# Kernel optimization log

Measured on AMD Instinct MI355X. Metric: run time of the kernel, lower is better.

The kernel has to match this reference:

```python
import jax, jax.numpy as jnp
import numpy as np

T, N, E = 2048, 11, 110
NF, EF, HID, EED, HEADS = 5, 4, 256, 32, 4
D1 = 64 * HEADS  # gat1 output dim = 256
BN_EPS = 1e-5
LN_EPS = 1e-5


def _gat(x, ea, src, dst, W, b, Wa, ba):
    """FallbackGAT: linear, gather src/dst, edge-score, softmax over ALL edges, scatter-add."""
    h = x @ W + b                                             # (N, D)
    sh, dh = h[src], h[dst]                                   # (E, D) gathers
    logits = jnp.concatenate([sh, dh, ea], axis=-1) @ Wa + ba # (E,)
    alpha = jax.nn.softmax(logits)                            # softmax over dim=0 (all edges), as in source
    return jax.ops.segment_sum(alpha[:, None] * sh, dst, num_segments=x.shape[0])


def _forward(x, edge_attr, event_embs, hx, edge_index,
             W_np, b_np, bn_g, bn_b,
             We1, be1, We2, be2,
             Wg1, bg1, Wa1, ba1,
             Wg2, bg2, Wa2, ba2,
             ln_g, ln_b,
             W_ih, W_hh, b_ih, b_hh,
             Wf, bf, Wp1, bp1, Wp2, bp2):
    src, dst = edge_index[0], edge_index[1]
    bn_inv = 1.0 / jnp.sqrt(1.0 + BN_EPS)  # eval-mode BatchNorm with running stats (0, 1)

    def step(h_state, inp):
        xt, eat, evt = inp  # (N,NF), (E,EF), (EED,)
        # node_proj: Linear -> ReLU -> BatchNorm1d (eval)
        h = jax.nn.relu(xt @ W_np + b_np)
        h = bn_g * (h * bn_inv) + bn_b
        # edge_proj: Linear -> ReLU -> Linear -> ReLU
        ea = jax.nn.relu(jax.nn.relu(eat @ We1 + be1) @ We2 + be2)
        # two GAT layers (dropout p=0)
        x1 = jax.nn.relu(_gat(h, ea, src, dst, Wg1, bg1, Wa1, ba1))
        x2 = jax.nn.relu(_gat(x1, ea, src, dst, Wg2, bg2, Wa2, ba2))
        # LayerNorm
        mu = x2.mean(-1, keepdims=True)
        var = ((x2 - mu) ** 2).mean(-1, keepdims=True)
        x2 = ln_g * (x2 - mu) / jnp.sqrt(var + LN_EPS) + ln_b
        # GRUCell (torch gate order r, z, n)
        gi = x2 @ W_ih + b_ih
        gh = h_state @ W_hh + b_hh
        ir, iz, inn = jnp.split(gi, 3, axis=-1)
        hr, hz, hn = jnp.split(gh, 3, axis=-1)
        r = jax.nn.sigmoid(ir + hr)
        z = jax.nn.sigmoid(iz + hz)
        n = jnp.tanh(inn + r * hn)
        h_new = (1.0 - z) * n + z * h_state
        # event fusion + predictor
        ev = jnp.broadcast_to(evt[None, :], (h_new.shape[0], evt.shape[0]))
        fused = jax.nn.relu(jnp.concatenate([h_new, ev], axis=-1) @ Wf + bf)
        pred = jax.nn.relu(fused @ Wp1 + bp1) @ Wp2 + bp2  # (N, 1)
        return h_new, pred

    _, preds = jax.lax.scan(step, hx, (x, edge_attr, event_embs))
    return preds  # (T, N, 1)


def setup_inputs() -> dict:
    key = jax.random.key(0)
    ks = jax.random.split(key, 20)
    def p(i, shape):
        return jax.random.normal(ks[i], shape, dtype=jnp.float32) * 0.05
    return dict(
        x=jax.random.normal(ks[0], (T, N, NF), dtype=jnp.float32),
        edge_attr=jax.random.uniform(ks[1], (T, E, EF), dtype=jnp.float32),
        event_embs=jax.random.normal(ks[2], (T, EED), dtype=jnp.float32),
        hx=jnp.zeros((N, HID), jnp.float32),
        edge_index=jax.random.randint(ks[3], (2, E), 0, N),
        W_np=p(4, (NF, 64)), b_np=jnp.zeros((64,), jnp.float32),
        bn_g=jnp.ones((64,), jnp.float32), bn_b=jnp.zeros((64,), jnp.float32),
        We1=p(5, (EF, 32)), be1=jnp.zeros((32,), jnp.float32),
        We2=p(6, (32, 16)), be2=jnp.zeros((16,), jnp.float32),
        Wg1=p(7, (64, D1)), bg1=jnp.zeros((D1,), jnp.float32),
        Wa1=p(8, (2 * D1 + 16,)), ba1=jnp.zeros((), jnp.float32),
        Wg2=p(9, (D1, HID)), bg2=jnp.zeros((HID,), jnp.float32),
        Wa2=p(10, (2 * HID + 16,)), ba2=jnp.zeros((), jnp.float32),
        ln_g=jnp.ones((HID,), jnp.float32), ln_b=jnp.zeros((HID,), jnp.float32),
        W_ih=p(11, (HID, 3 * HID)), W_hh=p(12, (HID, 3 * HID)),
        b_ih=jnp.zeros((3 * HID,), jnp.float32), b_hh=jnp.zeros((3 * HID,), jnp.float32),
        Wf=p(13, (HID + EED, HID)), bf=jnp.zeros((HID,), jnp.float32),
        Wp1=p(14, (HID, HID // 2)), bp1=jnp.zeros((HID // 2,), jnp.float32),
        Wp2=p(15, (HID // 2, 1)), bp2=jnp.zeros((1,), jnp.float32),
    )


def reference(x, edge_attr, event_embs, hx, edge_index,
              W_np, b_np, bn_g, bn_b,
              We1, be1, We2, be2,
              Wg1, bg1, Wa1, ba1,
              Wg2, bg2, Wa2, ba2,
              ln_g, ln_b,
              W_ih, W_hh, b_ih, b_hh,
              Wf, bf, Wp1, bp1, Wp2, bp2):
    return _forward(x, edge_attr, event_embs, hx, edge_index,
                    W_np, b_np, bn_g, bn_b,
                    We1, be1, We2, be2,
                    Wg1, bg1, Wa1, ba1,
                    Wg2, bg2, Wa2, ba2,
                    ln_g, ln_b,
                    W_ih, W_hh, b_ih, b_hh,
                    Wf, bf, Wp1, bp1, Wp2, bp2)
```

## Files before the change

kernel.cpp:

```cpp
#include <hip/hip_runtime.h>
#include <hip/hip_bf16.h>

#define TT   2048
#define NN   11
#define EE   110
#define NFD  5
#define EFD  4
#define HIDD 256
#define EEDD 32
#define DD1  256
#define G3   768
#define HPAD 264

typedef __attribute__((ext_vector_type(8))) short short8v;
typedef __attribute__((ext_vector_type(4))) float float4v;

static __device__ inline short f2bf(float f) {
    union { __hip_bfloat16 b; short s; } u; u.b = __float2bfloat16(f); return u.s;
}
static __device__ inline float bf2f(short s) {
    union { short s; __hip_bfloat16 b; } u; u.s = s; return __bfloat162float(u.b);
}
static __device__ inline float sigm_f(float x) {
    return __builtin_amdgcn_rcpf(1.f + __builtin_amdgcn_exp2f(-1.4426950408889634f * x));
}
static __device__ inline float tanh_f(float x) {
    float e = __builtin_amdgcn_exp2f(2.8853900817779268f * x);
    return 1.f - 2.f * __builtin_amdgcn_rcpf(e + 1.f);
}
static __device__ inline void gld16(const float* g, float* s) {
    __builtin_amdgcn_global_load_lds((const __attribute__((address_space(1))) void*)g,
                                     (__attribute__((address_space(3))) void*)s, 16, 0, 0);
}

__global__ __launch_bounds__(256) void precompute_kernel(
    const float* __restrict__ x, const float* __restrict__ edge_attr,
    const float* __restrict__ evs, const int* __restrict__ eidx,
    const float* __restrict__ W_np, const float* __restrict__ b_np,
    const float* __restrict__ bn_g, const float* __restrict__ bn_b,
    const float* __restrict__ We1, const float* __restrict__ be1,
    const float* __restrict__ We2, const float* __restrict__ be2,
    const float* __restrict__ Wg1, const float* __restrict__ bg1,
    const float* __restrict__ Wa1, const float* __restrict__ ba1,
    const float* __restrict__ Wg2, const float* __restrict__ bg2,
    const float* __restrict__ Wa2, const float* __restrict__ ba2,
    const float* __restrict__ ln_g, const float* __restrict__ ln_b,
    const float* __restrict__ W_ih, const float* __restrict__ b_ih,
    const float* __restrict__ Wf, const float* __restrict__ bf_,
    float* __restrict__ gi_out, float* __restrict__ evc_out)
{
    const int t   = blockIdx.x;
    const int tid = threadIdx.x;

    __shared__ __align__(16) float sh_h[NN][64];
    __shared__ __align__(16) float sh_e1[EE][32];
    __shared__ __align__(16) float sh_ea[EE][16];
    __shared__ __align__(16) float sh_h1[NN][DD1];
    __shared__ __align__(16) float sh_x[NN][DD1];
    __shared__ float sxt[NN * NFD];
    __shared__ float sev[EEDD];
    __shared__ float seat[EE * EFD];
    __shared__ float red[356];
    __shared__ float sh_s1[NN], sh_d1[NN];
    __shared__ float sh_elog[EE], sh_logit[EE], sh_alpha[EE];
    __shared__ float sh_mu[NN], sh_rs[NN];
    __shared__ float sredv[2];
    __shared__ int s_src[EE], s_dst[EE];
    __shared__ int cnt[NN], deg_start[NN + 1], e_by_dst[EE];

    if (tid < NN * NFD) sxt[tid] = x[(size_t)t * NN * NFD + tid];
    if (tid < EEDD)     sev[tid] = evs[(size_t)t * EEDD + tid];
    for (int i = tid; i < EE * EFD; i += 256)
        seat[i] = edge_attr[(size_t)t * EE * EFD + i];
    if (tid < EE) { s_src[tid] = eidx[tid]; s_dst[tid] = eidx[EE + tid]; }
    if (tid < NN) cnt[tid] = 0;
    __syncthreads();
    if (tid < EE) atomicAdd(&cnt[s_dst[tid]], 1);
    __syncthreads();
    if (tid == 0) {
        int a = 0;
        for (int n = 0; n < NN; n++) { deg_start[n] = a; a += cnt[n]; }
        deg_start[NN] = a;
    }
    __syncthreads();
    if (tid < NN) cnt[tid] = 0;
    __syncthreads();
    if (tid < EE) {
        int d = s_dst[tid];
        int pos = deg_start[d] + atomicAdd(&cnt[d], 1);
        e_by_dst[pos] = tid;
    }

    const float bn_inv = 1.0f / sqrtf(1.0f + 1e-5f);
    __syncthreads();
    for (int i = tid; i < NN * 64; i += 256) {
        int n = i >> 6, d = i & 63;
        float a = b_np[d];
        #pragma unroll
        for (int k = 0; k < NFD; k++) a += sxt[n * NFD + k] * W_np[k * 64 + d];
        a = fmaxf(a, 0.f);
        sh_h[n][d] = bn_g[d] * (a * bn_inv) + bn_b[d];
    }
    __syncthreads();

    for (int i = tid; i < EE * 32; i += 256) {
        int e = i >> 5, d = i & 31;
        float a = be1[d];
        #pragma unroll
        for (int k = 0; k < EFD; k++) a += seat[e * EFD + k] * We1[k * 32 + d];
        sh_e1[e][d] = fmaxf(a, 0.f);
    }
    __syncthreads();
    for (int i = tid; i < EE * 16; i += 256) {
        int e = i >> 4, d = i & 15;
        float a = be2[d];
        #pragma unroll
        for (int k = 0; k < 32; k++) a += sh_e1[e][k] * We2[k * 16 + d];
        sh_ea[e][d] = fmaxf(a, 0.f);
    }
    __syncthreads();

    {
        const int j = tid;
        float acc[NN];
        #pragma unroll
        for (int n = 0; n < NN; n++) acc[n] = bg1[j];
        for (int k = 0; k < 64; k += 4) {
            float w0 = Wg1[(k + 0) * DD1 + j], w1 = Wg1[(k + 1) * DD1 + j];
            float w2 = Wg1[(k + 2) * DD1 + j], w3 = Wg1[(k + 3) * DD1 + j];
            #pragma unroll
            for (int n = 0; n < NN; n++) {
                float4 hv = *(const float4*)&sh_h[n][k];
                acc[n] = fmaf(hv.w, w3, fmaf(hv.z, w2, fmaf(hv.y, w1, fmaf(hv.x, w0, acc[n]))));
            }
        }
        #pragma unroll
        for (int n = 0; n < NN; n++) sh_h1[n][j] = acc[n];
    }
    __syncthreads();
    if (tid < EE) {
        float a = ba1[0];
        #pragma unroll
        for (int k = 0; k < 16; k++) a += sh_ea[tid][k] * Wa1[2 * DD1 + k];
        sh_elog[tid] = a;
    }
    if (tid < 176) {
        int g = tid >> 3, jj = tid & 7;
        int n = (g < NN) ? g : (g - NN);
        const float* wa = (g < NN) ? Wa1 : (Wa1 + DD1);
        float s = 0.f;
        for (int k = jj; k < DD1; k += 8) s += sh_h1[n][k] * wa[k];
        red[tid] = s;
    }
    __syncthreads();
    if (tid < 22) {
        float s = 0.f;
        #pragma unroll
        for (int j2 = 0; j2 < 8; j2++) s += red[tid * 8 + j2];
        if (tid < NN) sh_s1[tid] = s; else sh_d1[tid - NN] = s;
    }
    __syncthreads();
    if (tid < EE) sh_logit[tid] = sh_s1[s_src[tid]] + sh_d1[s_dst[tid]] + sh_elog[tid];
    __syncthreads();
    if (tid < 128) red[tid] = (tid < EE) ? sh_logit[tid] : -3.0e38f;
    __syncthreads();
    for (int s = 64; s > 0; s >>= 1) {
        if (tid < s) red[tid] = fmaxf(red[tid], red[tid + s]);
        __syncthreads();
    }
    if (tid == 0) sredv[0] = red[0];
    __syncthreads();
    if (tid < 128) {
        float v = (tid < EE) ? expf(sh_logit[tid] - sredv[0]) : 0.f;
        if (tid < EE) sh_alpha[tid] = v;
        red[tid] = v;
    }
    __syncthreads();
    for (int s = 64; s > 0; s >>= 1) {
        if (tid < s) red[tid] += red[tid + s];
        __syncthreads();
    }
    if (tid == 0) sredv[1] = 1.f / red[0];
    __syncthreads();
    if (tid < EE) sh_alpha[tid] *= sredv[1];
    __syncthreads();
    for (int i = tid; i < NN * DD1; i += 256) {
        int n = i >> 8, d = i & 255;
        float a = 0.f;
        for (int p = deg_start[n]; p < deg_start[n + 1]; p++) {
            int e = e_by_dst[p];
            a += sh_alpha[e] * sh_h1[s_src[e]][d];
        }
        sh_x[n][d] = fmaxf(a, 0.f);
    }
    __syncthreads();

    {
        const int j = tid;
        float acc[NN];
        #pragma unroll
        for (int n = 0; n < NN; n++) acc[n] = bg2[j];
        for (int k = 0; k < DD1; k += 4) {
            float w0 = Wg2[(k + 0) * DD1 + j], w1 = Wg2[(k + 1) * DD1 + j];
            float w2 = Wg2[(k + 2) * DD1 + j], w3 = Wg2[(k + 3) * DD1 + j];
            #pragma unroll
            for (int n = 0; n < NN; n++) {
                float4 xv = *(const float4*)&sh_x[n][k];
                acc[n] = fmaf(xv.w, w3, fmaf(xv.z, w2, fmaf(xv.y, w1, fmaf(xv.x, w0, acc[n]))));
            }
        }
        #pragma unroll
        for (int n = 0; n < NN; n++) sh_h1[n][j] = acc[n];
    }
    __syncthreads();
    if (tid < EE) {
        float a = ba2[0];
        #pragma unroll
        for (int k = 0; k < 16; k++) a += sh_ea[tid][k] * Wa2[2 * DD1 + k];
        sh_elog[tid] = a;
    }
    if (tid < 176) {
        int g = tid >> 3, jj = tid & 7;
        int n = (g < NN) ? g : (g - NN);
        const float* wa = (g < NN) ? Wa2 : (Wa2 + DD1);
        float s = 0.f;
        for (int k = jj; k < DD1; k += 8) s += sh_h1[n][k] * wa[k];
        red[tid] = s;
    }
    __syncthreads();
    if (tid < 22) {
        float s = 0.f;
        #pragma unroll
        for (int j2 = 0; j2 < 8; j2++) s += red[tid * 8 + j2];
        if (tid < NN) sh_s1[tid] = s; else sh_d1[tid - NN] = s;
    }
    __syncthreads();
    if (tid < EE) sh_logit[tid] = sh_s1[s_src[tid]] + sh_d1[s_dst[tid]] + sh_elog[tid];
    __syncthreads();
    if (tid < 128) red[tid] = (tid < EE) ? sh_logit[tid] : -3.0e38f;
    __syncthreads();
    for (int s = 64; s > 0; s >>= 1) {
        if (tid < s) red[tid] = fmaxf(red[tid], red[tid + s]);
        __syncthreads();
    }
    if (tid == 0) sredv[0] = red[0];
    __syncthreads();
    if (tid < 128) {
        float v = (tid < EE) ? expf(sh_logit[tid] - sredv[0]) : 0.f;
        if (tid < EE) sh_alpha[tid] = v;
        red[tid] = v;
    }
    __syncthreads();
    for (int s = 64; s > 0; s >>= 1) {
        if (tid < s) red[tid] += red[tid + s];
        __syncthreads();
    }
    if (tid == 0) sredv[1] = 1.f / red[0];
    __syncthreads();
    if (tid < EE) sh_alpha[tid] *= sredv[1];
    __syncthreads();
    for (int i = tid; i < NN * DD1; i += 256) {
        int n = i >> 8, d = i & 255;
        float a = 0.f;
        for (int p = deg_start[n]; p < deg_start[n + 1]; p++) {
            int e = e_by_dst[p];
            a += sh_alpha[e] * sh_h1[s_src[e]][d];
        }
        sh_x[n][d] = fmaxf(a, 0.f);
    }
    __syncthreads();

    if (tid < 176) {
        int n = tid >> 4, jj = tid & 15;
        float s = 0.f, q = 0.f;
        for (int k = jj; k < DD1; k += 16) {
            float v = sh_x[n][k];
            s += v; q += v * v;
        }
        red[tid] = s; red[176 + tid] = q;
    }
    __syncthreads();
    if (tid < NN) {
        float s = 0.f, q = 0.f;
        #pragma unroll
        for (int j2 = 0; j2 < 16; j2++) { s += red[tid * 16 + j2]; q += red[176 + tid * 16 + j2]; }
        float mu = s * (1.f / 256.f);
        float var = q * (1.f / 256.f) - mu * mu;
        sh_mu[tid] = mu;
        sh_rs[tid] = 1.f / sqrtf(var + 1e-5f);
    }
    __syncthreads();
    for (int i = tid; i < NN * DD1; i += 256) {
        int n = i >> 8, d = i & 255;
        sh_x[n][d] = ln_g[d] * (sh_x[n][d] - sh_mu[n]) * sh_rs[n] + ln_b[d];
    }
    __syncthreads();

    #pragma unroll
    for (int c = 0; c < 3; c++) {
        const int j = tid + c * 256;
        float acc[NN];
        float bj = b_ih[j];
        #pragma unroll
        for (int n = 0; n < NN; n++) acc[n] = bj;
        for (int k = 0; k < HIDD; k += 4) {
            float w0 = W_ih[(size_t)(k + 0) * G3 + j], w1 = W_ih[(size_t)(k + 1) * G3 + j];
            float w2 = W_ih[(size_t)(k + 2) * G3 + j], w3 = W_ih[(size_t)(k + 3) * G3 + j];
            #pragma unroll
            for (int n = 0; n < NN; n++) {
                float4 xv = *(const float4*)&sh_x[n][k];
                acc[n] = fmaf(xv.w, w3, fmaf(xv.z, w2, fmaf(xv.y, w1, fmaf(xv.x, w0, acc[n]))));
            }
        }
        #pragma unroll
        for (int n = 0; n < NN; n++)
            gi_out[(size_t)t * NN * G3 + n * G3 + j] = acc[n];
    }

    {
        float a = bf_[tid];
        #pragma unroll
        for (int k = 0; k < EEDD; k++) a += sev[k] * Wf[(size_t)(HIDD + k) * HIDD + tid];
        evc_out[(size_t)t * HIDD + tid] = a;
    }
}

__global__ __launch_bounds__(512, 2) void scan_mfma_kernel(
    const float* __restrict__ gi, const float* __restrict__ W_hh,
    const float* __restrict__ b_hh, const float* __restrict__ hx,
    float* __restrict__ h_all)
{
    const int tid = threadIdx.x;
    const int w  = tid >> 6;
    const int l  = tid & 63;
    const int lc = l & 15;
    const int lg = l >> 4;

    __shared__ short sh_hi[2][16 * HPAD];
    __shared__ short sh_lo[2][16 * HPAD];
    __shared__ float sgi[2][NN * G3];

    {
        short* p0 = &sh_hi[0][0];
        short* p1 = &sh_lo[0][0];
        for (int i = tid; i < 2 * 16 * HPAD; i += 512) { p0[i] = 0; p1[i] = 0; }
    }

    short8v wf[48];
    float* wstage = &sgi[0][0];
    #pragma unroll
    for (int blk = 0; blk < 16; blk++) {
        __syncthreads();
        for (int i = tid; i < 16 * G3; i += 512)
            wstage[i] = W_hh[(size_t)(blk * 16) * G3 + i];
        __syncthreads();
        const int kk = blk >> 1, half = blk & 1;
        if ((lg >> 1) == half) {
            const int rbase = lg * 8 - half * 16;
            #pragma unroll
            for (int g = 0; g < 3; g++)
            #pragma unroll
            for (int f = 0; f < 2; f++) {
                const int col = g * 256 + w * 32 + f * 16 + lc;
                short8v v;
                #pragma unroll
                for (int j = 0; j < 8; j++)
                    v[j] = f2bf(wstage[(rbase + j) * G3 + col]);
                wf[kk * 6 + g * 2 + f] = v;
            }
        }
    }
    __syncthreads();

    float bias[6];
    #pragma unroll
    for (int g = 0; g < 3; g++)
    #pragma unroll
    for (int f = 0; f < 2; f++)
        bias[g * 2 + f] = b_hh[g * 256 + w * 32 + f * 16 + lc];

    float hreg[8];
    #pragma unroll
    for (int f = 0; f < 2; f++) {
        const int u = w * 32 + f * 16 + lc;
        #pragma unroll
        for (int q = 0; q < 4; q++) {
            const int n = lg * 4 + q;
            if (n < NN) {
                float h0 = hx[n * HIDD + u];
                hreg[f * 4 + q] = h0;
                short hi = f2bf(h0);
                sh_hi[0][n * HPAD + u] = hi;
                sh_lo[0][n * HPAD + u] = f2bf(h0 - bf2f(hi));
            }
        }
    }

    for (int c = w; c < 33; c += 8)
        gld16(gi + c * 256 + l * 4, &sgi[0][c * 256]);
    __syncthreads();

    for (int t = 0; t < TT; t++) {
        const int pb = t & 1, nb = pb ^ 1;

        if (t + 1 < TT) {
            const float* gsrc = gi + (size_t)(t + 1) * (NN * G3);
            for (int c = w; c < 33; c += 8)
                gld16(gsrc + c * 256 + l * 4, &sgi[nb][c * 256]);
        }

        const short* hbh = &sh_hi[pb][0];
        const short* hbl = &sh_lo[pb][0];
        float4v acc[6];
        #pragma unroll
        for (int j = 0; j < 6; j++)
            acc[j] = (float4v){bias[j], bias[j], bias[j], bias[j]};
        #pragma unroll
        for (int kk = 0; kk < 8; kk++) {
            const int ko = kk * 32 + lg * 8;
            short8v ahi = *(const short8v*)&hbh[lc * HPAD + ko];
            short8v alo = *(const short8v*)&hbl[lc * HPAD + ko];
            #pragma unroll
            for (int j = 0; j < 6; j++)
                acc[j] = __builtin_amdgcn_mfma_f32_16x16x32_bf16(ahi, wf[kk * 6 + j], acc[j], 0, 0, 0);
            #pragma unroll
            for (int j = 0; j < 6; j++)
                acc[j] = __builtin_amdgcn_mfma_f32_16x16x32_bf16(alo, wf[kk * 6 + j], acc[j], 0, 0, 0);
        }

        const float* gicur = &sgi[pb][0];
        short* nhi = &sh_hi[nb][0];
        short* nlo = &sh_lo[nb][0];
        #pragma unroll
        for (int f = 0; f < 2; f++) {
            const int u = w * 32 + f * 16 + lc;
            #pragma unroll
            for (int q = 0; q < 4; q++) {
                const int n = lg * 4 + q;
                if (n < NN) {
                    float gir = gicur[n * G3 + u];
                    float giz = gicur[n * G3 + 256 + u];
                    float gin = gicur[n * G3 + 512 + u];
                    float r   = sigm_f(gir + acc[f][q]);
                    float z   = sigm_f(giz + acc[2 + f][q]);
                    float nn_ = tanh_f(gin + r * acc[4 + f][q]);
                    float hnew = z * hreg[f * 4 + q] + (1.f - z) * nn_;
                    hreg[f * 4 + q] = hnew;
                    short hi = f2bf(hnew);
                    nhi[n * HPAD + u] = hi;
                    nlo[n * HPAD + u] = f2bf(hnew - bf2f(hi));
                    h_all[(size_t)t * (NN * HIDD) + n * HIDD + u] = hnew;
                }
            }
        }
        __syncthreads();
    }
}

__global__ __launch_bounds__(256) void predict_kernel(
    const float* __restrict__ h_all, const float* __restrict__ evc,
    const float* __restrict__ Wf, const float* __restrict__ Wp1,
    const float* __restrict__ bp1, const float* __restrict__ Wp2,
    const float* __restrict__ bp2, float* __restrict__ out)
{
    const int t = blockIdx.x, tid = threadIdx.x;
    __shared__ __align__(16) float sh[NN][HIDD];
    __shared__ __align__(16) float sf[NN][HIDD];
    __shared__ __align__(16) float sp[NN][128];
    __shared__ float red[176];

    for (int i = tid; i < NN * HIDD; i += 256)
        sh[i >> 8][i & 255] = h_all[(size_t)t * NN * HIDD + i];
    __syncthreads();
    {
        const int j = tid;
        float acc[NN];
        float e = evc[(size_t)t * HIDD + j];
        #pragma unroll
        for (int n = 0; n < NN; n++) acc[n] = e;
        for (int k = 0; k < HIDD; k += 4) {
            float w0 = Wf[(size_t)(k + 0) * HIDD + j], w1 = Wf[(size_t)(k + 1) * HIDD + j];
            float w2 = Wf[(size_t)(k + 2) * HIDD + j], w3 = Wf[(size_t)(k + 3) * HIDD + j];
            #pragma unroll
            for (int n = 0; n < NN; n++) {
                float4 hv = *(const float4*)&sh[n][k];
                acc[n] = fmaf(hv.w, w3, fmaf(hv.z, w2, fmaf(hv.y, w1, fmaf(hv.x, w0, acc[n]))));
            }
        }
        #pragma unroll
        for (int n = 0; n < NN; n++) sf[n][j] = fmaxf(acc[n], 0.f);
    }
    __syncthreads();
    if (tid < 128) {
        float acc[NN];
        float b = bp1[tid];
        #pragma unroll
        for (int n = 0; n < NN; n++) acc[n] = b;
        for (int k = 0; k < HIDD; k += 4) {
            float w0 = Wp1[(size_t)(k + 0) * 128 + tid], w1 = Wp1[(size_t)(k + 1) * 128 + tid];
            float w2 = Wp1[(size_t)(k + 2) * 128 + tid], w3 = Wp1[(size_t)(k + 3) * 128 + tid];
            #pragma unroll
            for (int n = 0; n < NN; n++) {
                float4 fv = *(const float4*)&sf[n][k];
                acc[n] = fmaf(fv.w, w3, fmaf(fv.z, w2, fmaf(fv.y, w1, fmaf(fv.x, w0, acc[n]))));
            }
        }
        #pragma unroll
        for (int n = 0; n < NN; n++) sp[n][tid] = fmaxf(acc[n], 0.f);
    }
    __syncthreads();
    if (tid < 176) {
        int n = tid >> 4, jj = tid & 15;
        float s = 0.f;
        for (int k = jj; k < 128; k += 16) s += sp[n][k] * Wp2[k];
        red[tid] = s;
    }
    __syncthreads();
    if (tid < NN) {
        float s = 0.f;
        #pragma unroll
        for (int j2 = 0; j2 < 16; j2++) s += red[tid * 16 + j2];
        out[(size_t)t * NN + tid] = s + bp2[0];
    }
}

extern "C" void kernel_launch(void* const* d_in, const int* in_sizes, int n_in,
                              void* d_out, int out_size, void* d_ws, size_t ws_size,
                              hipStream_t stream) {
    const float* x_in  = (const float*)d_in[0];
    const float* ea_in = (const float*)d_in[1];
    const float* evs   = (const float*)d_in[2];
    const float* hx    = (const float*)d_in[3];
    const int*   eidx  = (const int*)d_in[4];
    const float* W_np  = (const float*)d_in[5];
    const float* b_np  = (const float*)d_in[6];
    const float* bn_g  = (const float*)d_in[7];
    const float* bn_b  = (const float*)d_in[8];
    const float* We1   = (const float*)d_in[9];
    const float* be1   = (const float*)d_in[10];
    const float* We2   = (const float*)d_in[11];
    const float* be2   = (const float*)d_in[12];
    const float* Wg1   = (const float*)d_in[13];
    const float* bg1   = (const float*)d_in[14];
    const float* Wa1   = (const float*)d_in[15];
    const float* ba1   = (const float*)d_in[16];
    const float* Wg2   = (const float*)d_in[17];
    const float* bg2   = (const float*)d_in[18];
    const float* Wa2   = (const float*)d_in[19];
    const float* ba2   = (const float*)d_in[20];
    const float* ln_g  = (const float*)d_in[21];
    const float* ln_b  = (const float*)d_in[22];
    const float* W_ih  = (const float*)d_in[23];
    const float* W_hh  = (const float*)d_in[24];
    const float* b_ih  = (const float*)d_in[25];
    const float* b_hh  = (const float*)d_in[26];
    const float* Wf    = (const float*)d_in[27];
    const float* bf_   = (const float*)d_in[28];
    const float* Wp1   = (const float*)d_in[29];
    const float* bp1   = (const float*)d_in[30];
    const float* Wp2   = (const float*)d_in[31];
    const float* bp2   = (const float*)d_in[32];

    float* gi   = (float*)d_ws;
    float* evc  = gi  + (size_t)TT * NN * G3;
    float* hall = evc + (size_t)TT * HIDD;

    precompute_kernel<<<TT, 256, 0, stream>>>(
        x_in, ea_in, evs, eidx,
        W_np, b_np, bn_g, bn_b, We1, be1, We2, be2,
        Wg1, bg1, Wa1, ba1, Wg2, bg2, Wa2, ba2,
        ln_g, ln_b, W_ih, b_ih, Wf, bf_, gi, evc);

    scan_mfma_kernel<<<1, 512, 0, stream>>>(gi, W_hh, b_hh, hx, hall);

    predict_kernel<<<TT, 256, 0, stream>>>(
        hall, evc, Wf, Wp1, bp1, Wp2, bp2, (float*)d_out);
}
```

Before: 12.13 ms.

## Store gate inputs and hidden history in fp16 and relax scan barrier waits

Precomputed input-gate activations and the per-step hidden-state history are stored as fp16 instead of fp32. This halves the per-step global-to-LDS traffic in the serial single-block scan and the h_all write and read traffic. The scan's full __syncthreads is replaced by a barrier that waits only on LDS, leaving the prefetch of the next step's inputs in flight, and the MFMA section runs at raised wave priority. This costs some precision in the gate inputs and the hidden states fed to the predictor, and relies on a hand-coded vmcnt count being correct.

```diff
diff --git a/kernel.cpp b/kernel.cpp
--- a/kernel.cpp
+++ b/kernel.cpp
@@ -1,5 +1,6 @@
 #include <hip/hip_runtime.h>
 #include <hip/hip_bf16.h>
+#include <hip/hip_fp16.h>
 
 #define TT   2048
 #define NN   11
@@ -11,6 +12,7 @@
 #define DD1  256
 #define G3   768
 #define HPAD 264
+#define GIP  8704
 
 typedef __attribute__((ext_vector_type(8))) short short8v;
 typedef __attribute__((ext_vector_type(4))) float float4v;
@@ -20,6 +22,12 @@
 }
 static __device__ inline float bf2f(short s) {
     union { short s; __hip_bfloat16 b; } u; u.s = s; return __bfloat162float(u.b);
+}
+static __device__ inline unsigned short f2h(float x) {
+    return __half_as_ushort(__float2half(x));
+}
+static __device__ inline float h2f(unsigned short v) {
+    return __half2float(__ushort_as_half(v));
 }
 static __device__ inline float sigm_f(float x) {
     return __builtin_amdgcn_rcpf(1.f + __builtin_amdgcn_exp2f(-1.4426950408889634f * x));
@@ -28,7 +36,7 @@
     float e = __builtin_amdgcn_exp2f(2.8853900817779268f * x);
     return 1.f - 2.f * __builtin_amdgcn_rcpf(e + 1.f);
 }
-static __device__ inline void gld16(const float* g, float* s) {
+static __device__ inline void gld16(const void* g, void* s) {
     __builtin_amdgcn_global_load_lds((const __attribute__((address_space(1))) void*)g,
                                      (__attribute__((address_space(3))) void*)s, 16, 0, 0);
 }
@@ -47,7 +55,7 @@
     const float* __restrict__ ln_g, const float* __restrict__ ln_b,
     const float* __restrict__ W_ih, const float* __restrict__ b_ih,
     const float* __restrict__ Wf, const float* __restrict__ bf_,
-    float* __restrict__ gi_out, float* __restrict__ evc_out)
+    unsigned short* __restrict__ gi_out, float* __restrict__ evc_out)
 {
     const int t   = blockIdx.x;
     const int tid = threadIdx.x;
@@ -314,7 +322,7 @@
         }
         #pragma unroll
         for (int n = 0; n < NN; n++)
-            gi_out[(size_t)t * NN * G3 + n * G3 + j] = acc[n];
+            gi_out[(size_t)t * GIP + n * G3 + j] = f2h(acc[n]);
     }
 
     {
@@ -326,9 +334,9 @@
 }
 
 __global__ __launch_bounds__(512, 2) void scan_mfma_kernel(
-    const float* __restrict__ gi, const float* __restrict__ W_hh,
+    const unsigned short* __restrict__ gi16, const float* __restrict__ W_hh,
     const float* __restrict__ b_hh, const float* __restrict__ hx,
-    float* __restrict__ h_all)
+    unsigned short* __restrict__ hall16)
 {
     const int tid = threadIdx.x;
     const int w  = tid >> 6;
@@ -336,18 +344,13 @@
     const int lc = l & 15;
     const int lg = l >> 4;
 
-    __shared__ short sh_hi[2][16 * HPAD];
-    __shared__ short sh_lo[2][16 * HPAD];
-    __shared__ float sgi[2][NN * G3];
-
-    {
-        short* p0 = &sh_hi[0][0];
-        short* p1 = &sh_lo[0][0];
-        for (int i = tid; i < 2 * 16 * HPAD; i += 512) { p0[i] = 0; p1[i] = 0; }
-    }
+    __shared__ __align__(16) char smem[68608];
+    short* sh_hi = (short*)smem;
+    short* sh_lo = (short*)(smem + 16896);
+    unsigned short* sgi = (unsigned short*)(smem + 33792);
+    float* wstage = (float*)smem;
 
     short8v wf[48];
-    float* wstage = &sgi[0][0];
     #pragma unroll
     for (int blk = 0; blk < 16; blk++) {
         __syncthreads();
@@ -379,6 +382,9 @@
     for (int f = 0; f < 2; f++)
         bias[g * 2 + f] = b_hh[g * 256 + w * 32 + f * 16 + lc];
 
+    for (int i = tid; i < 2 * 16 * HPAD; i += 512) { sh_hi[i] = 0; sh_lo[i] = 0; }
+    __syncthreads();
+
     float hreg[8];
     #pragma unroll
     for (int f = 0; f < 2; f++) {
@@ -390,31 +396,34 @@
                 float h0 = hx[n * HIDD + u];
                 hreg[f * 4 + q] = h0;
                 short hi = f2bf(h0);
-                sh_hi[0][n * HPAD + u] = hi;
-                sh_lo[0][n * HPAD + u] = f2bf(h0 - bf2f(hi));
-            }
-        }
-    }
-
-    for (int c = w; c < 33; c += 8)
-        gld16(gi + c * 256 + l * 4, &sgi[0][c * 256]);
-    __syncthreads();
-
+                sh_hi[n * HPAD + u] = hi;
+                sh_lo[n * HPAD + u] = f2bf(h0 - bf2f(hi));
+            }
+        }
+    }
+
+    for (int c = w; c < 17; c += 8)
+        gld16(gi16 + c * 512 + l * 8, sgi + c * 512);
+    __syncthreads();
+
+    size_t hall_base = 0;
     for (int t = 0; t < TT; t++) {
         const int pb = t & 1, nb = pb ^ 1;
 
         if (t + 1 < TT) {
-            const float* gsrc = gi + (size_t)(t + 1) * (NN * G3);
-            for (int c = w; c < 33; c += 8)
-                gld16(gsrc + c * 256 + l * 4, &sgi[nb][c * 256]);
-        }
-
-        const short* hbh = &sh_hi[pb][0];
-        const short* hbl = &sh_lo[pb][0];
+            const unsigned short* gsrc = gi16 + (size_t)(t + 1) * GIP;
+            for (int c = w; c < 17; c += 8)
+                gld16(gsrc + c * 512 + l * 8, sgi + nb * GIP + c * 512);
+        }
+        __builtin_amdgcn_sched_barrier(0);
+
+        const short* hbh = sh_hi + pb * 16 * HPAD;
+        const short* hbl = sh_lo + pb * 16 * HPAD;
         float4v acc[6];
         #pragma unroll
         for (int j = 0; j < 6; j++)
             acc[j] = (float4v){bias[j], bias[j], bias[j], bias[j]};
+        __builtin_amdgcn_s_setprio(1);
         #pragma unroll
         for (int kk = 0; kk < 8; kk++) {
             const int ko = kk * 32 + lg * 8;
@@ -427,10 +436,11 @@
             for (int j = 0; j < 6; j++)
                 acc[j] = __builtin_amdgcn_mfma_f32_16x16x32_bf16(alo, wf[kk * 6 + j], acc[j], 0, 0, 0);
         }
-
-        const float* gicur = &sgi[pb][0];
-        short* nhi = &sh_hi[nb][0];
-        short* nlo = &sh_lo[nb][0];
+        __builtin_amdgcn_s_setprio(0);
+
+        const unsigned short* gic = sgi + pb * GIP;
+        short* nhi = sh_hi + nb * 16 * HPAD;
+        short* nlo = sh_lo + nb * 16 * HPAD;
         #pragma unroll
         for (int f = 0; f < 2; f++) {
             const int u = w * 32 + f * 16 + lc;
@@ -438,9 +448,9 @@
             for (int q = 0; q < 4; q++) {
                 const int n = lg * 4 + q;
                 if (n < NN) {
-                    float gir = gicur[n * G3 + u];
-                    float giz = gicur[n * G3 + 256 + u];
-                    float gin = gicur[n * G3 + 512 + u];
+                    float gir = h2f(gic[n * G3 + u]);
+                    float giz = h2f(gic[n * G3 + 256 + u]);
+                    float gin = h2f(gic[n * G3 + 512 + u]);
                     float r   = sigm_f(gir + acc[f][q]);
                     float z   = sigm_f(giz + acc[2 + f][q]);
                     float nn_ = tanh_f(gin + r * acc[4 + f][q]);
@@ -449,16 +459,21 @@
                     short hi = f2bf(hnew);
                     nhi[n * HPAD + u] = hi;
                     nlo[n * HPAD + u] = f2bf(hnew - bf2f(hi));
-                    h_all[(size_t)t * (NN * HIDD) + n * HIDD + u] = hnew;
+                    hall16[hall_base + n * HIDD + u] = f2h(hnew);
                 }
             }
         }
-        __syncthreads();
+
+        asm volatile("s_waitcnt vmcnt(8) lgkmcnt(0)" ::: "memory");
+        __builtin_amdgcn_s_barrier();
+        __builtin_amdgcn_sched_barrier(0);
+
+        hall_base += NN * HIDD;
     }
 }
 
 __global__ __launch_bounds__(256) void predict_kernel(
-    const float* __restrict__ h_all, const float* __restrict__ evc,
+    const unsigned short* __restrict__ hall16, const float* __restrict__ evc,
     const float* __restrict__ Wf, const float* __restrict__ Wp1,
     const float* __restrict__ bp1, const float* __restrict__ Wp2,
     const float* __restrict__ bp2, float* __restrict__ out)
@@ -470,7 +485,7 @@
     __shared__ float red[176];
 
     for (int i = tid; i < NN * HIDD; i += 256)
-        sh[i >> 8][i & 255] = h_all[(size_t)t * NN * HIDD + i];
+        sh[i >> 8][i & 255] = h2f(hall16[(size_t)t * NN * HIDD + i]);
     __syncthreads();
     {
         const int j = tid;
@@ -561,18 +576,18 @@
     const float* Wp2   = (const float*)d_in[31];
     const float* bp2   = (const float*)d_in[32];
 
-    float* gi   = (float*)d_ws;
-    float* evc  = gi  + (size_t)TT * NN * G3;
-    float* hall = evc + (size_t)TT * HIDD;
+    unsigned short* gi16 = (unsigned short*)d_ws;
+    float* evc = (float*)((char*)d_ws + (size_t)TT * GIP * 2);
+    unsigned short* hall16 = (unsigned short*)((char*)evc + (size_t)TT * HIDD * 4);
 
     precompute_kernel<<<TT, 256, 0, stream>>>(
         x_in, ea_in, evs, eidx,
         W_np, b_np, bn_g, bn_b, We1, be1, We2, be2,
         Wg1, bg1, Wa1, ba1, Wg2, bg2, Wa2, ba2,
-        ln_g, ln_b, W_ih, b_ih, Wf, bf_, gi, evc);
-
-    scan_mfma_kernel<<<1, 512, 0, stream>>>(gi, W_hh, b_hh, hx, hall);
+        ln_g, ln_b, W_ih, b_ih, Wf, bf_, gi16, evc);
+
+    scan_mfma_kernel<<<1, 512, 0, stream>>>(gi16, W_hh, b_hh, hx, hall16);
 
     predict_kernel<<<TT, 256, 0, stream>>>(
-        hall, evc, Wf, Wp1, bp1, Wp2, bp2, (float*)d_out);
-}
+        hall16, evc, Wf, Wp1, bp1, Wp2, bp2, (float*)d_out);
+}
```

Result: faster. 11.80 ms (-2.7%).

## Store GRU input gates fp16 in scan-thread layout and load directly to registers

Applied to the files above, without the earlier changes.

The precompute kernel now writes the input-gate projections as fp16, permuted so each scan thread reads its own 24 contiguous values. The serial scan kernel loads them straight into registers instead of double-buffering through LDS with global_load_lds. The hidden-state history is also stored as fp16. The per-step barrier becomes a bare lgkmcnt wait plus s_barrier, and the MFMA section runs at raised wave priority. The aim is to shrink memory traffic and LDS work on the single-block serial critical path, at the cost of fp16 rounding on gates and hidden states and an exposed global-load latency each step.

```diff
diff --git a/kernel.cpp b/kernel.cpp
--- a/kernel.cpp
+++ b/kernel.cpp
@@ -1,5 +1,6 @@
 #include <hip/hip_runtime.h>
 #include <hip/hip_bf16.h>
+#include <hip/hip_fp16.h>
 
 #define TT   2048
 #define NN   11
@@ -11,8 +12,11 @@
 #define DD1  256
 #define G3   768
 #define HPAD 264
+#define GPT  12288
 
 typedef __attribute__((ext_vector_type(8))) short short8v;
+typedef __attribute__((ext_vector_type(8))) unsigned short ushort8v;
+typedef __attribute__((ext_vector_type(4))) unsigned short ushort4v;
 typedef __attribute__((ext_vector_type(4))) float float4v;
 
 static __device__ inline short f2bf(float f) {
@@ -20,6 +24,12 @@
 }
 static __device__ inline float bf2f(short s) {
     union { short s; __hip_bfloat16 b; } u; u.s = s; return __bfloat162float(u.b);
+}
+static __device__ inline unsigned short f2h(float x) {
+    return __half_as_ushort(__float2half(x));
+}
+static __device__ inline float h2f(unsigned short v) {
+    return __half2float(__ushort_as_half(v));
 }
 static __device__ inline float sigm_f(float x) {
     return __builtin_amdgcn_rcpf(1.f + __builtin_amdgcn_exp2f(-1.4426950408889634f * x));
@@ -27,10 +37,6 @@
 static __device__ inline float tanh_f(float x) {
     float e = __builtin_amdgcn_exp2f(2.8853900817779268f * x);
     return 1.f - 2.f * __builtin_amdgcn_rcpf(e + 1.f);
-}
-static __device__ inline void gld16(const float* g, float* s) {
-    __builtin_amdgcn_global_load_lds((const __attribute__((address_space(1))) void*)g,
-                                     (__attribute__((address_space(3))) void*)s, 16, 0, 0);
 }
 
 __global__ __launch_bounds__(256) void precompute_kernel(
@@ -47,7 +53,7 @@
     const float* __restrict__ ln_g, const float* __restrict__ ln_b,
     const float* __restrict__ W_ih, const float* __restrict__ b_ih,
     const float* __restrict__ Wf, const float* __restrict__ bf_,
-    float* __restrict__ gi_out, float* __restrict__ evc_out)
+    unsigned short* __restrict__ gi_out, float* __restrict__ evc_out)
 {
     const int t   = blockIdx.x;
     const int tid = threadIdx.x;
@@ -296,25 +302,38 @@
     }
     __syncthreads();
 
-    #pragma unroll
-    for (int c = 0; c < 3; c++) {
-        const int j = tid + c * 256;
-        float acc[NN];
-        float bj = b_ih[j];
-        #pragma unroll
-        for (int n = 0; n < NN; n++) acc[n] = bj;
-        for (int k = 0; k < HIDD; k += 4) {
-            float w0 = W_ih[(size_t)(k + 0) * G3 + j], w1 = W_ih[(size_t)(k + 1) * G3 + j];
-            float w2 = W_ih[(size_t)(k + 2) * G3 + j], w3 = W_ih[(size_t)(k + 3) * G3 + j];
-            #pragma unroll
-            for (int n = 0; n < NN; n++) {
-                float4 xv = *(const float4*)&sh_x[n][k];
-                acc[n] = fmaf(xv.w, w3, fmaf(xv.z, w2, fmaf(xv.y, w1, fmaf(xv.x, w0, acc[n]))));
-            }
-        }
-        #pragma unroll
-        for (int n = 0; n < NN; n++)
-            gi_out[(size_t)t * NN * G3 + n * G3 + j] = acc[n];
+    {
+        const int wq  = tid >> 5;
+        const int fq  = (tid >> 4) & 1;
+        const int lcq = tid & 15;
+        #pragma unroll
+        for (int c = 0; c < 3; c++) {
+            const int j = tid + c * 256;
+            float acc[NN];
+            float bj = b_ih[j];
+            #pragma unroll
+            for (int n = 0; n < NN; n++) acc[n] = bj;
+            for (int k = 0; k < HIDD; k += 4) {
+                float w0 = W_ih[(size_t)(k + 0) * G3 + j], w1 = W_ih[(size_t)(k + 1) * G3 + j];
+                float w2 = W_ih[(size_t)(k + 2) * G3 + j], w3 = W_ih[(size_t)(k + 3) * G3 + j];
+                #pragma unroll
+                for (int n = 0; n < NN; n++) {
+                    float4 xv = *(const float4*)&sh_x[n][k];
+                    acc[n] = fmaf(xv.w, w3, fmaf(xv.z, w2, fmaf(xv.y, w1, fmaf(xv.x, w0, acc[n]))));
+                }
+            }
+            #pragma unroll
+            for (int lgq = 0; lgq < 3; lgq++) {
+                ushort4v v4;
+                #pragma unroll
+                for (int q = 0; q < 4; q++) {
+                    const int n = lgq * 4 + q;
+                    v4[q] = (n < NN) ? f2h(acc[n < NN ? n : 0]) : (unsigned short)0;
+                }
+                const int st = wq * 64 + lgq * 16 + lcq;
+                *(ushort4v*)(gi_out + (size_t)t * GPT + st * 24 + c * 8 + fq * 4) = v4;
+            }
+        }
     }
 
     {
@@ -326,9 +345,9 @@
 }
 
 __global__ __launch_bounds__(512, 2) void scan_mfma_kernel(
-    const float* __restrict__ gi, const float* __restrict__ W_hh,
+    const unsigned short* __restrict__ gip, const float* __restrict__ W_hh,
     const float* __restrict__ b_hh, const float* __restrict__ hx,
-    float* __restrict__ h_all)
+    unsigned short* __restrict__ hall16)
 {
     const int tid = threadIdx.x;
     const int w  = tid >> 6;
@@ -338,7 +357,7 @@
 
     __shared__ short sh_hi[2][16 * HPAD];
     __shared__ short sh_lo[2][16 * HPAD];
-    __shared__ float sgi[2][NN * G3];
+    __shared__ __align__(16) float wstage[16 * G3];
 
     {
         short* p0 = &sh_hi[0][0];
@@ -347,7 +366,6 @@
     }
 
     short8v wf[48];
-    float* wstage = &sgi[0][0];
     #pragma unroll
     for (int blk = 0; blk < 16; blk++) {
         __syncthreads();
@@ -370,7 +388,6 @@
             }
         }
     }
-    __syncthreads();
 
     float bias[6];
     #pragma unroll
@@ -395,19 +412,16 @@
             }
         }
     }
-
-    for (int c = w; c < 33; c += 8)
-        gld16(gi + c * 256 + l * 4, &sgi[0][c * 256]);
-    __syncthreads();
-
+    __syncthreads();
+
+    size_t hall_base = 0;
     for (int t = 0; t < TT; t++) {
         const int pb = t & 1, nb = pb ^ 1;
 
-        if (t + 1 < TT) {
-            const float* gsrc = gi + (size_t)(t + 1) * (NN * G3);
-            for (int c = w; c < 33; c += 8)
-                gld16(gsrc + c * 256 + l * 4, &sgi[nb][c * 256]);
-        }
+        const unsigned short* gp = gip + (size_t)t * GPT + tid * 24;
+        ushort8v ga = *(const ushort8v*)(gp);
+        ushort8v gb = *(const ushort8v*)(gp + 8);
+        ushort8v gc = *(const ushort8v*)(gp + 16);
 
         const short* hbh = &sh_hi[pb][0];
         const short* hbl = &sh_lo[pb][0];
@@ -415,6 +429,7 @@
         #pragma unroll
         for (int j = 0; j < 6; j++)
             acc[j] = (float4v){bias[j], bias[j], bias[j], bias[j]};
+        __builtin_amdgcn_s_setprio(1);
         #pragma unroll
         for (int kk = 0; kk < 8; kk++) {
             const int ko = kk * 32 + lg * 8;
@@ -427,8 +442,8 @@
             for (int j = 0; j < 6; j++)
                 acc[j] = __builtin_amdgcn_mfma_f32_16x16x32_bf16(alo, wf[kk * 6 + j], acc[j], 0, 0, 0);
         }
-
-        const float* gicur = &sgi[pb][0];
+        __builtin_amdgcn_s_setprio(0);
+
         short* nhi = &sh_hi[nb][0];
         short* nlo = &sh_lo[nb][0];
         #pragma unroll
@@ -438,9 +453,9 @@
             for (int q = 0; q < 4; q++) {
                 const int n = lg * 4 + q;
                 if (n < NN) {
-                    float gir = gicur[n * G3 + u];
-                    float giz = gicur[n * G3 + 256 + u];
-                    float gin = gicur[n * G3 + 512 + u];
+                    float gir = h2f(ga[f * 4 + q]);
+                    float giz = h2f(gb[f * 4 + q]);
+                    float gin = h2f(gc[f * 4 + q]);
                     float r   = sigm_f(gir + acc[f][q]);
                     float z   = sigm_f(giz + acc[2 + f][q]);
                     float nn_ = tanh_f(gin + r * acc[4 + f][q]);
@@ -449,16 +464,18 @@
                     short hi = f2bf(hnew);
                     nhi[n * HPAD + u] = hi;
                     nlo[n * HPAD + u] = f2bf(hnew - bf2f(hi));
-                    h_all[(size_t)t * (NN * HIDD) + n * HIDD + u] = hnew;
+                    hall16[hall_base + n * HIDD + u] = f2h(hnew);
                 }
             }
         }
-        __syncthreads();
+
+        asm volatile("s_waitcnt lgkmcnt(0)\n\ts_barrier" ::: "memory");
+        hall_base += NN * HIDD;
     }
 }
 
 __global__ __launch_bounds__(256) void predict_kernel(
-    const float* __restrict__ h_all, const float* __restrict__ evc,
+    const unsigned short* __restrict__ hall16, const float* __restrict__ evc,
     const float* __restrict__ Wf, const float* __restrict__ Wp1,
     const float* __restrict__ bp1, const float* __restrict__ Wp2,
     const float* __restrict__ bp2, float* __restrict__ out)
@@ -470,7 +487,7 @@
     __shared__ float red[176];
 
     for (int i = tid; i < NN * HIDD; i += 256)
-        sh[i >> 8][i & 255] = h_all[(size_t)t * NN * HIDD + i];
+        sh[i >> 8][i & 255] = h2f(hall16[(size_t)t * NN * HIDD + i]);
     __syncthreads();
     {
         const int j = tid;
@@ -561,18 +578,18 @@
     const float* Wp2   = (const float*)d_in[31];
     const float* bp2   = (const float*)d_in[32];
 
-    float* gi   = (float*)d_ws;
-    float* evc  = gi  + (size_t)TT * NN * G3;
-    float* hall = evc + (size_t)TT * HIDD;
+    unsigned short* gip = (unsigned short*)d_ws;
+    float* evc = (float*)((char*)d_ws + (size_t)TT * GPT * 2);
+    unsigned short* hall16 = (unsigned short*)((char*)evc + (size_t)TT * HIDD * 4);
 
     precompute_kernel<<<TT, 256, 0, stream>>>(
         x_in, ea_in, evs, eidx,
         W_np, b_np, bn_g, bn_b, We1, be1, We2, be2,
         Wg1, bg1, Wa1, ba1, Wg2, bg2, Wa2, ba2,
-        ln_g, ln_b, W_ih, b_ih, Wf, bf_, gi, evc);
-
-    scan_mfma_kernel<<<1, 512, 0, stream>>>(gi, W_hh, b_hh, hx, hall);
+        ln_g, ln_b, W_ih, b_ih, Wf, bf_, gip, evc);
+
+    scan_mfma_kernel<<<1, 512, 0, stream>>>(gip, W_hh, b_hh, hx, hall16);
 
     predict_kernel<<<TT, 256, 0, stream>>>(
-        hall, evc, Wf, Wp1, bp1, Wp2, bp2, (float*)d_out);
-}
+        hall16, evc, Wf, Wp1, bp1, Wp2, bp2, (float*)d_out);
+}
```

New measurement: 11.26 ms. 1.08x faster.
